# Kernel optimization log

Measured on AMD Instinct MI355X. Metric: run time of the kernel, lower is better.

## Reference

```python
import jax, jax.numpy as jnp
import numpy as np

N, C, E, H, K, GH, L = 50000, 256, 800000, 64, 32, 64, 2
EPS = 1e-8
LN_EPS = 1e-5


def setup_inputs() -> dict:
    key = jax.random.key(0)
    ks = jax.random.split(key, 24)
    s = lambda fan_in: 1.0 / np.sqrt(fan_in)
    inp = {
        "x": jax.random.normal(ks[0], (N, C), jnp.float32),
        "src": jax.random.randint(ks[1], (E,), 0, N),
        "dst": jax.random.randint(ks[2], (E,), 0, N),
        "base_w": jax.random.uniform(ks[3], (E,), jnp.float32),
        # encoder: Linear(C,H) -> ReLU -> Linear(H,H) -> ReLU  (weights stored [in,out])
        "enc_w1": jax.random.normal(ks[4], (C, H), jnp.float32) * s(C),
        "enc_b1": jnp.zeros((H,), jnp.float32),
        "enc_w2": jax.random.normal(ks[5], (H, H), jnp.float32) * s(H),
        "enc_b2": jnp.zeros((H,), jnp.float32),
        # edge gate: Linear(2H, GH) -> ReLU -> Linear(GH, 1) -> sigmoid
        "gate_w1": jax.random.normal(ks[6], (2 * H, GH), jnp.float32) * s(2 * H),
        "gate_b1": jnp.zeros((GH,), jnp.float32),
        "gate_w2": jax.random.normal(ks[7], (GH, 1), jnp.float32) * 0.1,
        "gate_b2": jnp.full((1,), 2.0, jnp.float32),
        # per-layer update MLPs (stacked over L layers): Linear(H,H)->ReLU->Linear(H,H)
        "upd_w1": jax.random.normal(ks[8], (L, H, H), jnp.float32) * s(H),
        "upd_b1": jnp.zeros((L, H), jnp.float32),
        "upd_w2": jax.random.normal(ks[9], (L, H, H), jnp.float32) * s(H),
        "upd_b2": jnp.zeros((L, H), jnp.float32),
        # per-layer LayerNorm params
        "ln_g": jnp.ones((L, H), jnp.float32),
        "ln_b": jnp.zeros((L, H), jnp.float32),
        # node reliability logits
        "rho_raw": jax.random.normal(ks[10], (N,), jnp.float32) * 0.1,
        # toU head: Linear(H, K)
        "toU_w": jax.random.normal(ks[11], (H, K), jnp.float32) * 0.1,
        "toU_b": jnp.ones((K,), jnp.float32),
    }
    return inp


def reference(x, src, dst, base_w,
              enc_w1, enc_b1, enc_w2, enc_b2,
              gate_w1, gate_b1, gate_w2, gate_b2,
              upd_w1, upd_b1, upd_w2, upd_b2,
              ln_g, ln_b, rho_raw, toU_w, toU_b):
    relu = jax.nn.relu
    # node encoder
    h = relu(relu(x @ enc_w1 + enc_b1) @ enc_w2 + enc_b2)  # [N, H]
    rho = jax.nn.sigmoid(rho_raw)                          # [N]
    rho_e = rho[src] * rho[dst]                            # [E]
    for l in range(L):
        h_src = h[src]                                     # [E, H] gather
        h_dst = h[dst]                                     # [E, H] gather
        z = relu(jnp.concatenate([h_src, h_dst], axis=1) @ gate_w1 + gate_b1)
        gate = jax.nn.sigmoid((z @ gate_w2 + gate_b2)[:, 0])  # [E]
        w = base_w * gate * rho_e                           # [E]
        # weighted scatter-add aggregate with degree normalization
        m = jax.ops.segment_sum(w[:, None] * h_src, dst, num_segments=N)  # [N, H]
        deg = jax.ops.segment_sum(w, dst, num_segments=N)                 # [N]
        neigh = m / (deg[:, None] + EPS)
        u = relu(neigh @ upd_w1[l] + upd_b1[l]) @ upd_w2[l] + upd_b2[l]
        pre = h + u
        mean = jnp.mean(pre, axis=-1, keepdims=True)
        var = jnp.var(pre, axis=-1, keepdims=True)
        h = (pre - mean) / jnp.sqrt(var + LN_EPS) * ln_g[l] + ln_b[l]
    U = jax.nn.softplus(h @ toU_w + toU_b)                 # [N, K]
    return U
```

## Files before the change

### kernel.cpp

```cpp
#include <hip/hip_runtime.h>
#include <math.h>


typedef unsigned short ushort_t;
typedef __attribute__((ext_vector_type(8))) short bf16x8;
typedef __attribute__((ext_vector_type(4))) float f32x4;

__device__ __forceinline__ float bf2f(ushort_t u) {
    return __uint_as_float(((unsigned int)u) << 16);
}
__device__ __forceinline__ ushort_t f2bf(float f) {
    unsigned int x = __float_as_uint(f);
    unsigned int lsb = (x >> 16) & 1u;
    x += 0x7fffu + lsb;
    return (ushort_t)(x >> 16);
}

__global__ __launch_bounds__(256) void pack_kernel(
    const float* __restrict__ w1, const float* __restrict__ w2,
    const float* __restrict__ gw1, const float* __restrict__ uw1,
    const float* __restrict__ uw2, const float* __restrict__ tw,
    ushort_t* __restrict__ w1f, ushort_t* __restrict__ w2f,
    ushort_t* __restrict__ g1f, ushort_t* __restrict__ u1f,
    ushort_t* __restrict__ u2f, ushort_t* __restrict__ tuf) {
    int t = blockIdx.x * 256 + threadIdx.x;
    if (t < 16384) {
        int i = t & 7, l = (t >> 3) & 63, kb = (t >> 9) & 7, nt = t >> 12;
        int k = kb * 32 + (l >> 4) * 8 + i, n = nt * 16 + (l & 15);
        w1f[t] = f2bf(w1[(size_t)k * 64 + n]);
    }
    if (t < 4096) {
        int i = t & 7, l = (t >> 3) & 63, kb = (t >> 9) & 1, nt = t >> 10;
        int k = kb * 32 + (l >> 4) * 8 + i, n = nt * 16 + (l & 15);
        w2f[t] = f2bf(w2[(size_t)k * 64 + n]);
    }
    if (t < 8192) {
        int i = t & 7, l = (t >> 3) & 63, kb = (t >> 9) & 1, j = t >> 10;
        int part = j >> 2, nt = j & 3;
        int k = part * 64 + kb * 32 + (l >> 4) * 8 + i, n = nt * 16 + (l & 15);
        g1f[t] = f2bf(gw1[(size_t)k * 64 + n]);
    }
    if (t < 8192) {
        int i = t & 7, l = (t >> 3) & 63, kb = (t >> 9) & 1;
        int nt = (t >> 10) & 3, lay = t >> 12;
        int k = kb * 32 + (l >> 4) * 8 + i, n = nt * 16 + (l & 15);
        u1f[t] = f2bf(uw1[(size_t)lay * 4096 + (size_t)k * 64 + n]);
        u2f[t] = f2bf(uw2[(size_t)lay * 4096 + (size_t)k * 64 + n]);
    }
    if (t < 2048) {
        int i = t & 7, l = (t >> 3) & 63, kb = (t >> 9) & 1, nt = t >> 10;
        int k = kb * 32 + (l >> 4) * 8 + i, n = nt * 16 + (l & 15);
        tuf[t] = f2bf(tw[(size_t)k * 32 + n]);
    }
}

__global__ __launch_bounds__(256) void enc_kernel(
    const float* __restrict__ x, const ushort_t* __restrict__ w1f,
    const float* __restrict__ b1, const ushort_t* __restrict__ w2f,
    const float* __restrict__ b2, const ushort_t* __restrict__ g1f,
    const float* __restrict__ gb1,
    ushort_t* __restrict__ ahb, float* __restrict__ bbuf, int N) {
    __shared__ ushort_t xls[4][16][264];
    __shared__ ushort_t tls[4][16][72];
    const int tid  = threadIdx.x;
    const int lane = tid & 63;
    const int w    = tid >> 6;
    const int m    = lane & 15;
    const int g    = lane >> 4;
    const int rbase = blockIdx.x * 64;
    for (int p = tid; p < 64 * 64; p += 256) {
        int row = p >> 6, k4 = p & 63;
        int grow = rbase + row;
        float4 v = (grow < N) ? *(const float4*)(x + (size_t)grow * 256 + k4 * 4)
                              : make_float4(0.f, 0.f, 0.f, 0.f);
        unsigned int p0 = (unsigned int)f2bf(v.x) | ((unsigned int)f2bf(v.y) << 16);
        unsigned int p1 = (unsigned int)f2bf(v.z) | ((unsigned int)f2bf(v.w) << 16);
        *(uint2*)&xls[row >> 4][row & 15][k4 * 4] = make_uint2(p0, p1);
    }
    __syncthreads();
    f32x4 acc[4] = {{0,0,0,0},{0,0,0,0},{0,0,0,0},{0,0,0,0}};
    #pragma unroll
    for (int kb = 0; kb < 8; ++kb) {
        bf16x8 a = *(const bf16x8*)&xls[w][m][kb * 32 + g * 8];
        #pragma unroll
        for (int nt = 0; nt < 4; ++nt) {
            bf16x8 b = *(const bf16x8*)(w1f + (((size_t)nt * 8 + kb) * 64 + lane) * 8);
            acc[nt] = __builtin_amdgcn_mfma_f32_16x16x32_bf16(a, b, acc[nt], 0, 0, 0);
        }
    }
    #pragma unroll
    for (int nt = 0; nt < 4; ++nt) {
        float bb1 = b1[nt * 16 + m];
        #pragma unroll
        for (int r = 0; r < 4; ++r) {
            float tv = fmaxf(acc[nt][r] + bb1, 0.f);
            tls[w][g * 4 + r][nt * 16 + m] = f2bf(tv);
        }
    }
    f32x4 acc2[4] = {{0,0,0,0},{0,0,0,0},{0,0,0,0},{0,0,0,0}};
    #pragma unroll
    for (int kb = 0; kb < 2; ++kb) {
        bf16x8 a2 = *(const bf16x8*)&tls[w][m][kb * 32 + g * 8];
        #pragma unroll
        for (int nt = 0; nt < 4; ++nt) {
            bf16x8 b = *(const bf16x8*)(w2f + (((size_t)nt * 2 + kb) * 64 + lane) * 8);
            acc2[nt] = __builtin_amdgcn_mfma_f32_16x16x32_bf16(a2, b, acc2[nt], 0, 0, 0);
        }
    }
    #pragma unroll
    for (int nt = 0; nt < 4; ++nt) {
        float bb2 = b2[nt * 16 + m];
        #pragma unroll
        for (int r = 0; r < 4; ++r) {
            float hv = fmaxf(acc2[nt][r] + bb2, 0.f);
            int grow = rbase + w * 16 + g * 4 + r;
            ushort_t hb = f2bf(hv);
            tls[w][g * 4 + r][nt * 16 + m] = hb;
            if (grow < N)
                ahb[(size_t)grow * 128 + 64 + nt * 16 + m] = hb;
        }
    }
    f32x4 accp[8] = {{0,0,0,0},{0,0,0,0},{0,0,0,0},{0,0,0,0},
                     {0,0,0,0},{0,0,0,0},{0,0,0,0},{0,0,0,0}};
    #pragma unroll
    for (int kb = 0; kb < 2; ++kb) {
        bf16x8 a3 = *(const bf16x8*)&tls[w][m][kb * 32 + g * 8];
        #pragma unroll
        for (int j = 0; j < 8; ++j) {
            bf16x8 b = *(const bf16x8*)(g1f + (((size_t)j * 2 + kb) * 64 + lane) * 8);
            accp[j] = __builtin_amdgcn_mfma_f32_16x16x32_bf16(a3, b, accp[j], 0, 0, 0);
        }
    }
    #pragma unroll
    for (int nt = 0; nt < 4; ++nt) {
        float gbl = gb1[nt * 16 + m];
        #pragma unroll
        for (int r = 0; r < 4; ++r) {
            int grow = rbase + w * 16 + g * 4 + r;
            if (grow < N) {
                ahb[(size_t)grow * 128 + nt * 16 + m] = f2bf(accp[nt][r] + gbl);
                bbuf[(size_t)grow * 64 + nt * 16 + m] = accp[nt + 4][r];
            }
        }
    }
}

__global__ __launch_bounds__(256) void hist_kernel(
    const int* __restrict__ dst, int* __restrict__ cnt,
    int* __restrict__ rank, int E) {
    for (int e = blockIdx.x * blockDim.x + threadIdx.x; e < E;
         e += gridDim.x * blockDim.x)
        rank[e] = atomicAdd(&cnt[dst[e]], 1);
}

__global__ __launch_bounds__(256) void scan1_kernel(
    const int* __restrict__ cnt, int* __restrict__ bsum, int N) {
    __shared__ int red[256];
    int i = blockIdx.x * 256 + threadIdx.x;
    red[threadIdx.x] = (i < N) ? cnt[i] : 0;
    __syncthreads();
    for (int off = 128; off > 0; off >>= 1) {
        if (threadIdx.x < off) red[threadIdx.x] += red[threadIdx.x + off];
        __syncthreads();
    }
    if (threadIdx.x == 0) bsum[blockIdx.x] = red[0];
}

__global__ __launch_bounds__(1024) void scan2_kernel(
    int* __restrict__ bsum, int nb) {
    __shared__ int s[1024];
    int v = (threadIdx.x < nb) ? bsum[threadIdx.x] : 0;
    s[threadIdx.x] = v;
    __syncthreads();
    for (int off = 1; off < 1024; off <<= 1) {
        int t = (threadIdx.x >= off) ? s[threadIdx.x - off] : 0;
        __syncthreads();
        s[threadIdx.x] += t;
        __syncthreads();
    }
    if (threadIdx.x < nb) bsum[threadIdx.x] = s[threadIdx.x] - v;
}

__global__ __launch_bounds__(256) void scan3_kernel(
    const int* __restrict__ cnt, const int* __restrict__ bsum,
    int* __restrict__ row_ptr, int N) {
    __shared__ int s[256];
    int i = blockIdx.x * 256 + threadIdx.x;
    int v = (i < N) ? cnt[i] : 0;
    s[threadIdx.x] = v;
    __syncthreads();
    for (int off = 1; off < 256; off <<= 1) {
        int t = (threadIdx.x >= off) ? s[threadIdx.x - off] : 0;
        __syncthreads();
        s[threadIdx.x] += t;
        __syncthreads();
    }
    if (i < N) row_ptr[i] = bsum[blockIdx.x] + s[threadIdx.x] - v;
    if (i == N - 1) row_ptr[N] = bsum[blockIdx.x] + s[threadIdx.x];
}

__global__ __launch_bounds__(256) void scatter_kernel(
    const int* __restrict__ src, const int* __restrict__ dst,
    const float* __restrict__ base_w, const float* __restrict__ rr,
    const int* __restrict__ row_ptr, const int* __restrict__ rank,
    int2* __restrict__ recs, int E) {
    for (int e = blockIdx.x * blockDim.x + threadIdx.x; e < E;
         e += gridDim.x * blockDim.x) {
        int s = src[e], d = dst[e];
        int pos = row_ptr[d] + rank[e];
        float rs = 1.f / (1.f + __expf(-rr[s]));
        float rd = 1.f / (1.f + __expf(-rr[d]));
        float c = base_w[e] * rs * rd;
        recs[pos] = make_int2(s, __float_as_int(c));
    }
}

__global__ __launch_bounds__(256) void gateagg_kernel(
    const int* __restrict__ row_ptr, const int2* __restrict__ recs,
    const ushort_t* __restrict__ ahb, const float* __restrict__ bb,
    const float* __restrict__ gw2, const float* __restrict__ gb2,
    ushort_t* __restrict__ nb, int N) {
    const int lane = threadIdx.x & 63;
    const int sub  = lane & 15;
    const int grp  = lane >> 4;
    const float4 gv = ((const float4*)gw2)[sub];
    const float gb = gb2[0];
    const int wid  = blockIdx.x * (blockDim.x >> 6) + (threadIdx.x >> 6);
    const int nw   = gridDim.x * (blockDim.x >> 6);
    for (int n = wid; n < N; n += nw) {
        const int beg = row_ptr[n], end = row_ptr[n + 1];
        const float4 bv = *(const float4*)(bb + (size_t)n * 64 + sub * 4);
        float m0 = 0.f, m1 = 0.f, m2 = 0.f, m3 = 0.f, dacc = 0.f;
        int i = beg + grp;
        for (; i + 4 < end; i += 8) {
            int2 rA = recs[i];
            int2 rB = recs[i + 4];
            const ushort_t* rowA = ahb + (size_t)rA.x * 128;
            const ushort_t* rowB = ahb + (size_t)rB.x * 128;
            ushort4 avA = *(const ushort4*)(rowA + sub * 4);
            ushort4 hvA = *(const ushort4*)(rowA + 64 + sub * 4);
            ushort4 avB = *(const ushort4*)(rowB + sub * 4);
            ushort4 hvB = *(const ushort4*)(rowB + 64 + sub * 4);
            float tA = fmaxf(bf2f(avA.x) + bv.x, 0.f) * gv.x
                     + fmaxf(bf2f(avA.y) + bv.y, 0.f) * gv.y
                     + fmaxf(bf2f(avA.z) + bv.z, 0.f) * gv.z
                     + fmaxf(bf2f(avA.w) + bv.w, 0.f) * gv.w;
            float tB = fmaxf(bf2f(avB.x) + bv.x, 0.f) * gv.x
                     + fmaxf(bf2f(avB.y) + bv.y, 0.f) * gv.y
                     + fmaxf(bf2f(avB.z) + bv.z, 0.f) * gv.z
                     + fmaxf(bf2f(avB.w) + bv.w, 0.f) * gv.w;
            #pragma unroll
            for (int o = 8; o > 0; o >>= 1) {
                tA += __shfl_xor(tA, o, 64);
                tB += __shfl_xor(tB, o, 64);
            }
            float wA = __int_as_float(rA.y) / (1.f + __expf(-(tA + gb)));
            float wB = __int_as_float(rB.y) / (1.f + __expf(-(tB + gb)));
            m0 = fmaf(wA, bf2f(hvA.x), m0); m0 = fmaf(wB, bf2f(hvB.x), m0);
            m1 = fmaf(wA, bf2f(hvA.y), m1); m1 = fmaf(wB, bf2f(hvB.y), m1);
            m2 = fmaf(wA, bf2f(hvA.z), m2); m2 = fmaf(wB, bf2f(hvB.z), m2);
            m3 = fmaf(wA, bf2f(hvA.w), m3); m3 = fmaf(wB, bf2f(hvB.w), m3);
            dacc += wA + wB;
        }
        if (i < end) {
            int2 r = recs[i];
            const ushort_t* row = ahb + (size_t)r.x * 128;
            ushort4 av = *(const ushort4*)(row + sub * 4);
            ushort4 hv = *(const ushort4*)(row + 64 + sub * 4);
            float t = fmaxf(bf2f(av.x) + bv.x, 0.f) * gv.x
                    + fmaxf(bf2f(av.y) + bv.y, 0.f) * gv.y
                    + fmaxf(bf2f(av.z) + bv.z, 0.f) * gv.z
                    + fmaxf(bf2f(av.w) + bv.w, 0.f) * gv.w;
            #pragma unroll
            for (int o = 8; o > 0; o >>= 1) t += __shfl_xor(t, o, 64);
            float w = __int_as_float(r.y) / (1.f + __expf(-(t + gb)));
            m0 = fmaf(w, bf2f(hv.x), m0);
            m1 = fmaf(w, bf2f(hv.y), m1);
            m2 = fmaf(w, bf2f(hv.z), m2);
            m3 = fmaf(w, bf2f(hv.w), m3);
            dacc += w;
        }
        #pragma unroll
        for (int o = 16; o < 64; o <<= 1) {
            m0 += __shfl_xor(m0, o, 64);
            m1 += __shfl_xor(m1, o, 64);
            m2 += __shfl_xor(m2, o, 64);
            m3 += __shfl_xor(m3, o, 64);
            dacc += __shfl_xor(dacc, o, 64);
        }
        if (lane < 16) {
            float dg = dacc + 1e-8f;
            ushort4 o4;
            o4.x = f2bf(m0 / dg);
            o4.y = f2bf(m1 / dg);
            o4.z = f2bf(m2 / dg);
            o4.w = f2bf(m3 / dg);
            *(ushort4*)(nb + (size_t)n * 64 + sub * 4) = o4;
        }
    }
}

template <int MODE>
__global__ __launch_bounds__(256) void upd_kernel(
    const ushort_t* __restrict__ nb,
    const ushort_t* __restrict__ u1f, const float* __restrict__ b1,
    const ushort_t* __restrict__ u2f, const float* __restrict__ b2,
    const float* __restrict__ lng, const float* __restrict__ lnb,
    const ushort_t* __restrict__ g1f, const float* __restrict__ gb1,
    ushort_t* __restrict__ ahb, float* __restrict__ bbuf,
    const ushort_t* __restrict__ tuf, const float* __restrict__ tub,
    float* __restrict__ U, int N) {
    __shared__ ushort_t tls[4][16][72];
    const int tid  = threadIdx.x;
    const int lane = tid & 63;
    const int w    = tid >> 6;
    const int m_   = lane & 15;
    const int g    = lane >> 4;
    const int rbase = blockIdx.x * 64;
    const int arow = rbase + w * 16 + m_;
    const bool rowok = arow < N;
    f32x4 acc[4] = {{0,0,0,0},{0,0,0,0},{0,0,0,0},{0,0,0,0}};
    #pragma unroll
    for (int kb = 0; kb < 2; ++kb) {
        bf16x8 a = {0, 0, 0, 0, 0, 0, 0, 0};
        if (rowok) a = *(const bf16x8*)(nb + (size_t)arow * 64 + kb * 32 + g * 8);
        #pragma unroll
        for (int nt = 0; nt < 4; ++nt) {
            bf16x8 b = *(const bf16x8*)(u1f + (((size_t)nt * 2 + kb) * 64 + lane) * 8);
            acc[nt] = __builtin_amdgcn_mfma_f32_16x16x32_bf16(a, b, acc[nt], 0, 0, 0);
        }
    }
    #pragma unroll
    for (int nt = 0; nt < 4; ++nt) {
        float bb1 = b1[nt * 16 + m_];
        #pragma unroll
        for (int r = 0; r < 4; ++r)
            tls[w][g * 4 + r][nt * 16 + m_] = f2bf(fmaxf(acc[nt][r] + bb1, 0.f));
    }
    f32x4 acc2[4] = {{0,0,0,0},{0,0,0,0},{0,0,0,0},{0,0,0,0}};
    #pragma unroll
    for (int kb = 0; kb < 2; ++kb) {
        bf16x8 a2 = *(const bf16x8*)&tls[w][m_][kb * 32 + g * 8];
        #pragma unroll
        for (int nt = 0; nt < 4; ++nt) {
            bf16x8 b = *(const bf16x8*)(u2f + (((size_t)nt * 2 + kb) * 64 + lane) * 8);
            acc2[nt] = __builtin_amdgcn_mfma_f32_16x16x32_bf16(a2, b, acc2[nt], 0, 0, 0);
        }
    }
    float hn_reg[4][4];
    #pragma unroll
    for (int r = 0; r < 4; ++r) {
        const int grow = rbase + w * 16 + g * 4 + r;
        float pre[4];
        float s1 = 0.f, s2 = 0.f;
        #pragma unroll
        for (int nt = 0; nt < 4; ++nt) {
            float hv = (grow < N)
                ? bf2f(ahb[(size_t)grow * 128 + 64 + nt * 16 + m_]) : 0.f;
            pre[nt] = acc2[nt][r] + b2[nt * 16 + m_] + hv;
            s1 += pre[nt];
            s2 += pre[nt] * pre[nt];
        }
        #pragma unroll
        for (int o = 1; o < 16; o <<= 1) {
            s1 += __shfl_xor(s1, o, 64);
            s2 += __shfl_xor(s2, o, 64);
        }
        float mean = s1 * (1.0f / 64.0f);
        float var  = s2 * (1.0f / 64.0f) - mean * mean;
        float rinv = rsqrtf(var + 1e-5f);
        #pragma unroll
        for (int nt = 0; nt < 4; ++nt) {
            float hn = (pre[nt] - mean) * rinv * lng[nt * 16 + m_] + lnb[nt * 16 + m_];
            hn_reg[r][nt] = hn;
            tls[w][g * 4 + r][nt * 16 + m_] = f2bf(hn);
        }
    }
    if (MODE == 0) {
        #pragma unroll
        for (int nt = 0; nt < 4; ++nt) {
            #pragma unroll
            for (int r = 0; r < 4; ++r) {
                int grow = rbase + w * 16 + g * 4 + r;
                if (grow < N)
                    ahb[(size_t)grow * 128 + 64 + nt * 16 + m_] = f2bf(hn_reg[r][nt]);
            }
        }
        f32x4 accp[8] = {{0,0,0,0},{0,0,0,0},{0,0,0,0},{0,0,0,0},
                         {0,0,0,0},{0,0,0,0},{0,0,0,0},{0,0,0,0}};
        #pragma unroll
        for (int kb = 0; kb < 2; ++kb) {
            bf16x8 a3 = *(const bf16x8*)&tls[w][m_][kb * 32 + g * 8];
            #pragma unroll
            for (int j = 0; j < 8; ++j) {
                bf16x8 b = *(const bf16x8*)(g1f + (((size_t)j * 2 + kb) * 64 + lane) * 8);
                accp[j] = __builtin_amdgcn_mfma_f32_16x16x32_bf16(a3, b, accp[j], 0, 0, 0);
            }
        }
        #pragma unroll
        for (int nt = 0; nt < 4; ++nt) {
            float gbl = gb1[nt * 16 + m_];
            #pragma unroll
            for (int r = 0; r < 4; ++r) {
                int grow = rbase + w * 16 + g * 4 + r;
                if (grow < N) {
                    ahb[(size_t)grow * 128 + nt * 16 + m_] = f2bf(accp[nt][r] + gbl);
                    bbuf[(size_t)grow * 64 + nt * 16 + m_] = accp[nt + 4][r];
                }
            }
        }
    } else {
        f32x4 accu[2] = {{0,0,0,0},{0,0,0,0}};
        #pragma unroll
        for (int kb = 0; kb < 2; ++kb) {
            bf16x8 a3 = *(const bf16x8*)&tls[w][m_][kb * 32 + g * 8];
            #pragma unroll
            for (int nt = 0; nt < 2; ++nt) {
                bf16x8 b = *(const bf16x8*)(tuf + (((size_t)nt * 2 + kb) * 64 + lane) * 8);
                accu[nt] = __builtin_amdgcn_mfma_f32_16x16x32_bf16(a3, b, accu[nt], 0, 0, 0);
            }
        }
        #pragma unroll
        for (int nt = 0; nt < 2; ++nt) {
            float tb = tub[nt * 16 + m_];
            #pragma unroll
            for (int r = 0; r < 4; ++r) {
                int grow = rbase + w * 16 + g * 4 + r;
                if (grow < N) {
                    float av = accu[nt][r] + tb;
                    float sp = av > 0.f ? av + log1pf(__expf(-av))
                                        : log1pf(__expf(av));
                    U[(size_t)grow * 32 + nt * 16 + m_] = sp;
                }
            }
        }
    }
}

extern "C" void kernel_launch(void* const* d_in, const int* in_sizes, int n_in,
                              void* d_out, int out_size, void* d_ws, size_t ws_size,
                              hipStream_t stream) {
    const float* x       = (const float*)d_in[0];
    const int*   src     = (const int*)d_in[1];
    const int*   dst     = (const int*)d_in[2];
    const float* base_w  = (const float*)d_in[3];
    const float* enc_w1  = (const float*)d_in[4];
    const float* enc_b1  = (const float*)d_in[5];
    const float* enc_w2  = (const float*)d_in[6];
    const float* enc_b2  = (const float*)d_in[7];
    const float* gate_w1 = (const float*)d_in[8];
    const float* gate_b1 = (const float*)d_in[9];
    const float* gate_w2 = (const float*)d_in[10];
    const float* gate_b2 = (const float*)d_in[11];
    const float* upd_w1  = (const float*)d_in[12];
    const float* upd_b1  = (const float*)d_in[13];
    const float* upd_w2  = (const float*)d_in[14];
    const float* upd_b2  = (const float*)d_in[15];
    const float* ln_g    = (const float*)d_in[16];
    const float* ln_b    = (const float*)d_in[17];
    const float* rho_raw = (const float*)d_in[18];
    const float* toU_w   = (const float*)d_in[19];
    const float* toU_b   = (const float*)d_in[20];

    const int N = in_sizes[18];
    const int E = in_sizes[1];
    const int nsb = (N + 255) / 256;

    float* ws  = (float*)d_ws;
    size_t off = 0;
    ushort_t* ahb = (ushort_t*)(ws + off); off += (size_t)N * 64;
    float* bb  = ws + off; off += (size_t)N * 64;
    ushort_t* nb = (ushort_t*)(ws + off); off += (size_t)N * 32;
    int* row_ptr = (int*)(ws + off); off += (size_t)((N + 1 + 3) & ~3);
    int* cnt     = (int*)(ws + off); off += (size_t)((N + 3) & ~3);
    int* bsum    = (int*)(ws + off); off += (size_t)((nsb + 3) & ~3);
    int* rank    = (int*)(ws + off); off += (size_t)E;
    int2* recs   = (int2*)(ws + off); off += (size_t)E * 2;
    ushort_t* w1f = (ushort_t*)(ws + off); off += 8192;
    ushort_t* w2f = (ushort_t*)(ws + off); off += 2048;
    ushort_t* g1f = (ushort_t*)(ws + off); off += 4096;
    ushort_t* u1f = (ushort_t*)(ws + off); off += 4096;
    ushort_t* u2f = (ushort_t*)(ws + off); off += 4096;
    ushort_t* tuf = (ushort_t*)(ws + off); off += 1024;

    pack_kernel<<<64, 256, 0, stream>>>(enc_w1, enc_w2, gate_w1, upd_w1, upd_w2,
                                        toU_w, w1f, w2f, g1f, u1f, u2f, tuf);
    const int nblk64 = (N + 63) / 64;
    enc_kernel<<<nblk64, 256, 0, stream>>>(x, w1f, enc_b1, w2f, enc_b2,
                                           g1f, gate_b1, ahb, bb, N);

    hipMemsetAsync(cnt, 0, (size_t)N * sizeof(int), stream);
    hist_kernel<<<(E + 255) / 256, 256, 0, stream>>>(dst, cnt, rank, E);
    scan1_kernel<<<nsb, 256, 0, stream>>>(cnt, bsum, N);
    scan2_kernel<<<1, 1024, 0, stream>>>(bsum, nsb);
    scan3_kernel<<<nsb, 256, 0, stream>>>(cnt, bsum, row_ptr, N);
    scatter_kernel<<<(E + 255) / 256, 256, 0, stream>>>(src, dst, base_w, rho_raw,
                                                        row_ptr, rank, recs, E);

    gateagg_kernel<<<2048, 256, 0, stream>>>(row_ptr, recs, ahb, bb,
                                             gate_w2, gate_b2, nb, N);
    upd_kernel<0><<<nblk64, 256, 0, stream>>>(
        nb, u1f, upd_b1, u2f, upd_b2, ln_g, ln_b,
        g1f, gate_b1, ahb, bb, tuf, toU_b, (float*)d_out, N);

    gateagg_kernel<<<2048, 256, 0, stream>>>(row_ptr, recs, ahb, bb,
                                             gate_w2, gate_b2, nb, N);
    upd_kernel<1><<<nblk64, 256, 0, stream>>>(
        nb, u1f + 4096, upd_b1 + 64, u2f + 4096, upd_b2 + 64,
        ln_g + 64, ln_b + 64,
        g1f, gate_b1, ahb, bb, tuf, toU_b, (float*)d_out, N);
}
```

Baseline: 213.3 us.

## Split node tile across waves by output columns and stage stores through LDS

The encoder and update kernels now process 16 nodes per block instead of 64. Each of the four waves computes one 16-column slice of the output rather than a full 16-row tile, with LDS exchanges and block barriers between stages and a cross-wave LayerNorm reduction done through shared memory. Global writes of h, the gate projections and bbuf are staged through LDS so they go out as row-contiguous vector stores instead of scattered 2-byte stores. The intent is 4x more blocks for better occupancy and wider global stores. The cost is extra barriers, redundant A-operand LDS reads across waves, and W operands reloaded per block.

New measurement: 200.0 us. 6.2% less time.

```diff
diff --git a/kernel.cpp b/kernel.cpp
--- a/kernel.cpp
+++ b/kernel.cpp
@@ -60,87 +60,93 @@
     const float* __restrict__ b2, const ushort_t* __restrict__ g1f,
     const float* __restrict__ gb1,
     ushort_t* __restrict__ ahb, float* __restrict__ bbuf, int N) {
-    __shared__ ushort_t xls[4][16][264];
-    __shared__ ushort_t tls[4][16][72];
+    __shared__ ushort_t xls[16][264];
+    __shared__ ushort_t tls[16][72];
+    __shared__ ushort_t hls[16][72];
+    __shared__ ushort_t als[16][72];
+    __shared__ float    bls[16][68];
     const int tid  = threadIdx.x;
     const int lane = tid & 63;
     const int w    = tid >> 6;
     const int m    = lane & 15;
     const int g    = lane >> 4;
-    const int rbase = blockIdx.x * 64;
-    for (int p = tid; p < 64 * 64; p += 256) {
-        int row = p >> 6, k4 = p & 63;
-        int grow = rbase + row;
+    const int rbase = blockIdx.x * 16;
+    for (int p = tid; p < 16 * 64; p += 256) {
+        int row = p >> 6, k4 = p & 63, grow = rbase + row;
         float4 v = (grow < N) ? *(const float4*)(x + (size_t)grow * 256 + k4 * 4)
                               : make_float4(0.f, 0.f, 0.f, 0.f);
         unsigned int p0 = (unsigned int)f2bf(v.x) | ((unsigned int)f2bf(v.y) << 16);
         unsigned int p1 = (unsigned int)f2bf(v.z) | ((unsigned int)f2bf(v.w) << 16);
-        *(uint2*)&xls[row >> 4][row & 15][k4 * 4] = make_uint2(p0, p1);
-    }
-    __syncthreads();
-    f32x4 acc[4] = {{0,0,0,0},{0,0,0,0},{0,0,0,0},{0,0,0,0}};
+        *(uint2*)&xls[row][k4 * 4] = make_uint2(p0, p1);
+    }
+    __syncthreads();
+    f32x4 acc = {0, 0, 0, 0};
     #pragma unroll
     for (int kb = 0; kb < 8; ++kb) {
-        bf16x8 a = *(const bf16x8*)&xls[w][m][kb * 32 + g * 8];
-        #pragma unroll
-        for (int nt = 0; nt < 4; ++nt) {
-            bf16x8 b = *(const bf16x8*)(w1f + (((size_t)nt * 8 + kb) * 64 + lane) * 8);
-            acc[nt] = __builtin_amdgcn_mfma_f32_16x16x32_bf16(a, b, acc[nt], 0, 0, 0);
-        }
-    }
-    #pragma unroll
-    for (int nt = 0; nt < 4; ++nt) {
-        float bb1 = b1[nt * 16 + m];
-        #pragma unroll
-        for (int r = 0; r < 4; ++r) {
-            float tv = fmaxf(acc[nt][r] + bb1, 0.f);
-            tls[w][g * 4 + r][nt * 16 + m] = f2bf(tv);
-        }
-    }
-    f32x4 acc2[4] = {{0,0,0,0},{0,0,0,0},{0,0,0,0},{0,0,0,0}};
+        bf16x8 a = *(const bf16x8*)&xls[m][kb * 32 + g * 8];
+        bf16x8 b = *(const bf16x8*)(w1f + (((size_t)w * 8 + kb) * 64 + lane) * 8);
+        acc = __builtin_amdgcn_mfma_f32_16x16x32_bf16(a, b, acc, 0, 0, 0);
+    }
+    {
+        float bb1 = b1[w * 16 + m];
+        #pragma unroll
+        for (int r = 0; r < 4; ++r)
+            tls[g * 4 + r][w * 16 + m] = f2bf(fmaxf(acc[r] + bb1, 0.f));
+    }
+    __syncthreads();
+    f32x4 acc2 = {0, 0, 0, 0};
     #pragma unroll
     for (int kb = 0; kb < 2; ++kb) {
-        bf16x8 a2 = *(const bf16x8*)&tls[w][m][kb * 32 + g * 8];
-        #pragma unroll
-        for (int nt = 0; nt < 4; ++nt) {
-            bf16x8 b = *(const bf16x8*)(w2f + (((size_t)nt * 2 + kb) * 64 + lane) * 8);
-            acc2[nt] = __builtin_amdgcn_mfma_f32_16x16x32_bf16(a2, b, acc2[nt], 0, 0, 0);
-        }
-    }
-    #pragma unroll
-    for (int nt = 0; nt < 4; ++nt) {
-        float bb2 = b2[nt * 16 + m];
-        #pragma unroll
-        for (int r = 0; r < 4; ++r) {
-            float hv = fmaxf(acc2[nt][r] + bb2, 0.f);
-            int grow = rbase + w * 16 + g * 4 + r;
-            ushort_t hb = f2bf(hv);
-            tls[w][g * 4 + r][nt * 16 + m] = hb;
-            if (grow < N)
-                ahb[(size_t)grow * 128 + 64 + nt * 16 + m] = hb;
-        }
-    }
-    f32x4 accp[8] = {{0,0,0,0},{0,0,0,0},{0,0,0,0},{0,0,0,0},
-                     {0,0,0,0},{0,0,0,0},{0,0,0,0},{0,0,0,0}};
+        bf16x8 a2 = *(const bf16x8*)&tls[m][kb * 32 + g * 8];
+        bf16x8 b = *(const bf16x8*)(w2f + (((size_t)w * 2 + kb) * 64 + lane) * 8);
+        acc2 = __builtin_amdgcn_mfma_f32_16x16x32_bf16(a2, b, acc2, 0, 0, 0);
+    }
+    {
+        float bb2 = b2[w * 16 + m];
+        #pragma unroll
+        for (int r = 0; r < 4; ++r)
+            hls[g * 4 + r][w * 16 + m] = f2bf(fmaxf(acc2[r] + bb2, 0.f));
+    }
+    __syncthreads();
+    {
+        int row = tid >> 4, c4 = tid & 15, grow = rbase + row;
+        if (grow < N)
+            *(ushort4*)(ahb + (size_t)grow * 128 + 64 + c4 * 4) =
+                *(const ushort4*)&hls[row][c4 * 4];
+    }
+    f32x4 p0 = {0, 0, 0, 0}, p1 = {0, 0, 0, 0};
     #pragma unroll
     for (int kb = 0; kb < 2; ++kb) {
-        bf16x8 a3 = *(const bf16x8*)&tls[w][m][kb * 32 + g * 8];
-        #pragma unroll
-        for (int j = 0; j < 8; ++j) {
-            bf16x8 b = *(const bf16x8*)(g1f + (((size_t)j * 2 + kb) * 64 + lane) * 8);
-            accp[j] = __builtin_amdgcn_mfma_f32_16x16x32_bf16(a3, b, accp[j], 0, 0, 0);
-        }
-    }
-    #pragma unroll
-    for (int nt = 0; nt < 4; ++nt) {
-        float gbl = gb1[nt * 16 + m];
+        bf16x8 a3 = *(const bf16x8*)&hls[m][kb * 32 + g * 8];
+        bf16x8 b0 = *(const bf16x8*)(g1f + (((size_t)(2 * w) * 2 + kb) * 64 + lane) * 8);
+        bf16x8 b1v = *(const bf16x8*)(g1f + (((size_t)(2 * w + 1) * 2 + kb) * 64 + lane) * 8);
+        p0 = __builtin_amdgcn_mfma_f32_16x16x32_bf16(a3, b0, p0, 0, 0, 0);
+        p1 = __builtin_amdgcn_mfma_f32_16x16x32_bf16(a3, b1v, p1, 0, 0, 0);
+    }
+    if (w < 2) {
+        int j0 = 2 * w, j1 = 2 * w + 1;
+        float gb0 = gb1[j0 * 16 + m], gb1v = gb1[j1 * 16 + m];
         #pragma unroll
         for (int r = 0; r < 4; ++r) {
-            int grow = rbase + w * 16 + g * 4 + r;
-            if (grow < N) {
-                ahb[(size_t)grow * 128 + nt * 16 + m] = f2bf(accp[nt][r] + gbl);
-                bbuf[(size_t)grow * 64 + nt * 16 + m] = accp[nt + 4][r];
-            }
+            als[g * 4 + r][j0 * 16 + m] = f2bf(p0[r] + gb0);
+            als[g * 4 + r][j1 * 16 + m] = f2bf(p1[r] + gb1v);
+        }
+    } else {
+        int j0 = 2 * w - 4, j1 = 2 * w - 3;
+        #pragma unroll
+        for (int r = 0; r < 4; ++r) {
+            bls[g * 4 + r][j0 * 16 + m] = p0[r];
+            bls[g * 4 + r][j1 * 16 + m] = p1[r];
+        }
+    }
+    __syncthreads();
+    {
+        int row = tid >> 4, c4 = tid & 15, grow = rbase + row;
+        if (grow < N) {
+            *(ushort4*)(ahb + (size_t)grow * 128 + c4 * 4) =
+                *(const ushort4*)&als[row][c4 * 4];
+            *(float4*)(bbuf + (size_t)grow * 64 + c4 * 4) =
+                *(const float4*)&bls[row][c4 * 4];
         }
     }
 }
@@ -310,127 +316,144 @@
     ushort_t* __restrict__ ahb, float* __restrict__ bbuf,
     const ushort_t* __restrict__ tuf, const float* __restrict__ tub,
     float* __restrict__ U, int N) {
-    __shared__ ushort_t tls[4][16][72];
+    __shared__ ushort_t xn[16][72];
+    __shared__ ushort_t hls[16][72];
+    __shared__ ushort_t tls[16][72];
+    __shared__ ushort_t als[16][72];
+    __shared__ float    bls[16][68];
+    __shared__ float    sred[16][4][2];
     const int tid  = threadIdx.x;
     const int lane = tid & 63;
     const int w    = tid >> 6;
     const int m_   = lane & 15;
     const int g    = lane >> 4;
-    const int rbase = blockIdx.x * 64;
-    const int arow = rbase + w * 16 + m_;
-    const bool rowok = arow < N;
-    f32x4 acc[4] = {{0,0,0,0},{0,0,0,0},{0,0,0,0},{0,0,0,0}};
+    const int rbase = blockIdx.x * 16;
+    {
+        int row = tid >> 4, c4 = tid & 15, grow = rbase + row;
+        ushort4 z; z.x = z.y = z.z = z.w = 0;
+        ushort4 nv = (grow < N) ? *(const ushort4*)(nb + (size_t)grow * 64 + c4 * 4) : z;
+        ushort4 hv = (grow < N) ? *(const ushort4*)(ahb + (size_t)grow * 128 + 64 + c4 * 4) : z;
+        *(ushort4*)&xn[row][c4 * 4] = nv;
+        *(ushort4*)&hls[row][c4 * 4] = hv;
+    }
+    __syncthreads();
+    f32x4 acc = {0, 0, 0, 0};
     #pragma unroll
     for (int kb = 0; kb < 2; ++kb) {
-        bf16x8 a = {0, 0, 0, 0, 0, 0, 0, 0};
-        if (rowok) a = *(const bf16x8*)(nb + (size_t)arow * 64 + kb * 32 + g * 8);
-        #pragma unroll
-        for (int nt = 0; nt < 4; ++nt) {
-            bf16x8 b = *(const bf16x8*)(u1f + (((size_t)nt * 2 + kb) * 64 + lane) * 8);
-            acc[nt] = __builtin_amdgcn_mfma_f32_16x16x32_bf16(a, b, acc[nt], 0, 0, 0);
-        }
-    }
-    #pragma unroll
-    for (int nt = 0; nt < 4; ++nt) {
-        float bb1 = b1[nt * 16 + m_];
+        bf16x8 a = *(const bf16x8*)&xn[m_][kb * 32 + g * 8];
+        bf16x8 b = *(const bf16x8*)(u1f + (((size_t)w * 2 + kb) * 64 + lane) * 8);
+        acc = __builtin_amdgcn_mfma_f32_16x16x32_bf16(a, b, acc, 0, 0, 0);
+    }
+    {
+        float bb1 = b1[w * 16 + m_];
         #pragma unroll
         for (int r = 0; r < 4; ++r)
-            tls[w][g * 4 + r][nt * 16 + m_] = f2bf(fmaxf(acc[nt][r] + bb1, 0.f));
-    }
-    f32x4 acc2[4] = {{0,0,0,0},{0,0,0,0},{0,0,0,0},{0,0,0,0}};
+            tls[g * 4 + r][w * 16 + m_] = f2bf(fmaxf(acc[r] + bb1, 0.f));
+    }
+    __syncthreads();
+    f32x4 acc2 = {0, 0, 0, 0};
     #pragma unroll
     for (int kb = 0; kb < 2; ++kb) {
-        bf16x8 a2 = *(const bf16x8*)&tls[w][m_][kb * 32 + g * 8];
-        #pragma unroll
-        for (int nt = 0; nt < 4; ++nt) {
-            bf16x8 b = *(const bf16x8*)(u2f + (((size_t)nt * 2 + kb) * 64 + lane) * 8);
-            acc2[nt] = __builtin_amdgcn_mfma_f32_16x16x32_bf16(a2, b, acc2[nt], 0, 0, 0);
-        }
-    }
-    float hn_reg[4][4];
-    #pragma unroll
-    for (int r = 0; r < 4; ++r) {
-        const int grow = rbase + w * 16 + g * 4 + r;
-        float pre[4];
-        float s1 = 0.f, s2 = 0.f;
-        #pragma unroll
-        for (int nt = 0; nt < 4; ++nt) {
-            float hv = (grow < N)
-                ? bf2f(ahb[(size_t)grow * 128 + 64 + nt * 16 + m_]) : 0.f;
-            pre[nt] = acc2[nt][r] + b2[nt * 16 + m_] + hv;
-            s1 += pre[nt];
-            s2 += pre[nt] * pre[nt];
-        }
-        #pragma unroll
-        for (int o = 1; o < 16; o <<= 1) {
-            s1 += __shfl_xor(s1, o, 64);
-            s2 += __shfl_xor(s2, o, 64);
-        }
-        float mean = s1 * (1.0f / 64.0f);
-        float var  = s2 * (1.0f / 64.0f) - mean * mean;
-        float rinv = rsqrtf(var + 1e-5f);
-        #pragma unroll
-        for (int nt = 0; nt < 4; ++nt) {
-            float hn = (pre[nt] - mean) * rinv * lng[nt * 16 + m_] + lnb[nt * 16 + m_];
-            hn_reg[r][nt] = hn;
-            tls[w][g * 4 + r][nt * 16 + m_] = f2bf(hn);
-        }
-    }
+        bf16x8 a2 = *(const bf16x8*)&tls[m_][kb * 32 + g * 8];
+        bf16x8 b = *(const bf16x8*)(u2f + (((size_t)w * 2 + kb) * 64 + lane) * 8);
+        acc2 = __builtin_amdgcn_mfma_f32_16x16x32_bf16(a2, b, acc2, 0, 0, 0);
+    }
+    float pre[4];
+    {
+        float bb2 = b2[w * 16 + m_];
+        #pragma unroll
+        for (int r = 0; r < 4; ++r) {
+            pre[r] = acc2[r] + bb2 + bf2f(hls[g * 4 + r][w * 16 + m_]);
+            float s1 = pre[r], s2 = pre[r] * pre[r];
+            #pragma unroll
+            for (int o = 1; o < 16; o <<= 1) {
+                s1 += __shfl_xor(s1, o, 64);
+                s2 += __shfl_xor(s2, o, 64);
+            }
+            if (m_ == 0) {
+                sred[g * 4 + r][w][0] = s1;
+                sred[g * 4 + r][w][1] = s2;
+            }
+        }
+    }
+    __syncthreads();
+    {
+        float lg = lng[w * 16 + m_], lb = lnb[w * 16 + m_];
+        #pragma unroll
+        for (int r = 0; r < 4; ++r) {
+            int row = g * 4 + r;
+            float s1 = (sred[row][0][0] + sred[row][1][0])
+                     + (sred[row][2][0] + sred[row][3][0]);
+            float s2 = (sred[row][0][1] + sred[row][1][1])
+                     + (sred[row][2][1] + sred[row][3][1]);
+            float mean = s1 * (1.0f / 64.0f);
+            float var  = s2 * (1.0f / 64.0f) - mean * mean;
+            float rinv = rsqrtf(var + 1e-5f);
+            float hn = (pre[r] - mean) * rinv * lg + lb;
+            tls[row][w * 16 + m_] = f2bf(hn);
+        }
+    }
+    __syncthreads();
     if (MODE == 0) {
-        #pragma unroll
-        for (int nt = 0; nt < 4; ++nt) {
+        {
+            int row = tid >> 4, c4 = tid & 15, grow = rbase + row;
+            if (grow < N)
+                *(ushort4*)(ahb + (size_t)grow * 128 + 64 + c4 * 4) =
+                    *(const ushort4*)&tls[row][c4 * 4];
+        }
+        f32x4 p0 = {0, 0, 0, 0}, p1 = {0, 0, 0, 0};
+        #pragma unroll
+        for (int kb = 0; kb < 2; ++kb) {
+            bf16x8 a3 = *(const bf16x8*)&tls[m_][kb * 32 + g * 8];
+            bf16x8 b0 = *(const bf16x8*)(g1f + (((size_t)(2 * w) * 2 + kb) * 64 + lane) * 8);
+            bf16x8 b1v = *(const bf16x8*)(g1f + (((size_t)(2 * w + 1) * 2 + kb) * 64 + lane) * 8);
+            p0 = __builtin_amdgcn_mfma_f32_16x16x32_bf16(a3, b0, p0, 0, 0, 0);
+            p1 = __builtin_amdgcn_mfma_f32_16x16x32_bf16(a3, b1v, p1, 0, 0, 0);
+        }
+        if (w < 2) {
+            int j0 = 2 * w, j1 = 2 * w + 1;
+            float gb0 = gb1[j0 * 16 + m_], gb1v = gb1[j1 * 16 + m_];
             #pragma unroll
             for (int r = 0; r < 4; ++r) {
-                int grow = rbase + w * 16 + g * 4 + r;
-                if (grow < N)
-                    ahb[(size_t)grow * 128 + 64 + nt * 16 + m_] = f2bf(hn_reg[r][nt]);
-            }
-        }
-        f32x4 accp[8] = {{0,0,0,0},{0,0,0,0},{0,0,0,0},{0,0,0,0},
-                         {0,0,0,0},{0,0,0,0},{0,0,0,0},{0,0,0,0}};
-        #pragma unroll
-        for (int kb = 0; kb < 2; ++kb) {
-            bf16x8 a3 = *(const bf16x8*)&tls[w][m_][kb * 32 + g * 8];
-            #pragma unroll
-            for (int j = 0; j < 8; ++j) {
-                bf16x8 b = *(const bf16x8*)(g1f + (((size_t)j * 2 + kb) * 64 + lane) * 8);
-                accp[j] = __builtin_amdgcn_mfma_f32_16x16x32_bf16(a3, b, accp[j], 0, 0, 0);
-            }
-        }
-        #pragma unroll
-        for (int nt = 0; nt < 4; ++nt) {
-            float gbl = gb1[nt * 16 + m_];
+                als[g * 4 + r][j0 * 16 + m_] = f2bf(p0[r] + gb0);
+                als[g * 4 + r][j1 * 16 + m_] = f2bf(p1[r] + gb1v);
+            }
+        } else {
+            int j0 = 2 * w - 4, j1 = 2 * w - 3;
             #pragma unroll
             for (int r = 0; r < 4; ++r) {
-                int grow = rbase + w * 16 + g * 4 + r;
+                bls[g * 4 + r][j0 * 16 + m_] = p0[r];
+                bls[g * 4 + r][j1 * 16 + m_] = p1[r];
+            }
+        }
+        __syncthreads();
+        {
+            int row = tid >> 4, c4 = tid & 15, grow = rbase + row;
+            if (grow < N) {
+                *(ushort4*)(ahb + (size_t)grow * 128 + c4 * 4) =
+                    *(const ushort4*)&als[row][c4 * 4];
+                *(float4*)(bbuf + (size_t)grow * 64 + c4 * 4) =
+                    *(const float4*)&bls[row][c4 * 4];
+            }
+        }
+    } else {
+        if (w < 2) {
+            f32x4 au = {0, 0, 0, 0};
+            #pragma unroll
+            for (int kb = 0; kb < 2; ++kb) {
+                bf16x8 a3 = *(const bf16x8*)&tls[m_][kb * 32 + g * 8];
+                bf16x8 b = *(const bf16x8*)(tuf + (((size_t)w * 2 + kb) * 64 + lane) * 8);
+                au = __builtin_amdgcn_mfma_f32_16x16x32_bf16(a3, b, au, 0, 0, 0);
+            }
+            float tb = tub[w * 16 + m_];
+            #pragma unroll
+            for (int r = 0; r < 4; ++r) {
+                int grow = rbase + g * 4 + r;
                 if (grow < N) {
-                    ahb[(size_t)grow * 128 + nt * 16 + m_] = f2bf(accp[nt][r] + gbl);
-                    bbuf[(size_t)grow * 64 + nt * 16 + m_] = accp[nt + 4][r];
-                }
-            }
-        }
-    } else {
-        f32x4 accu[2] = {{0,0,0,0},{0,0,0,0}};
-        #pragma unroll
-        for (int kb = 0; kb < 2; ++kb) {
-            bf16x8 a3 = *(const bf16x8*)&tls[w][m_][kb * 32 + g * 8];
-            #pragma unroll
-            for (int nt = 0; nt < 2; ++nt) {
-                bf16x8 b = *(const bf16x8*)(tuf + (((size_t)nt * 2 + kb) * 64 + lane) * 8);
-                accu[nt] = __builtin_amdgcn_mfma_f32_16x16x32_bf16(a3, b, accu[nt], 0, 0, 0);
-            }
-        }
-        #pragma unroll
-        for (int nt = 0; nt < 2; ++nt) {
-            float tb = tub[nt * 16 + m_];
-            #pragma unroll
-            for (int r = 0; r < 4; ++r) {
-                int grow = rbase + w * 16 + g * 4 + r;
-                if (grow < N) {
-                    float av = accu[nt][r] + tb;
+                    float av = au[r] + tb;
                     float sp = av > 0.f ? av + log1pf(__expf(-av))
                                         : log1pf(__expf(av));
-                    U[(size_t)grow * 32 + nt * 16 + m_] = sp;
+                    U[(size_t)grow * 32 + w * 16 + m_] = sp;
                 }
             }
         }
@@ -485,8 +508,8 @@
 
     pack_kernel<<<64, 256, 0, stream>>>(enc_w1, enc_w2, gate_w1, upd_w1, upd_w2,
                                         toU_w, w1f, w2f, g1f, u1f, u2f, tuf);
-    const int nblk64 = (N + 63) / 64;
-    enc_kernel<<<nblk64, 256, 0, stream>>>(x, w1f, enc_b1, w2f, enc_b2,
+    const int nblk16 = (N + 15) / 16;
+    enc_kernel<<<nblk16, 256, 0, stream>>>(x, w1f, enc_b1, w2f, enc_b2,
                                            g1f, gate_b1, ahb, bb, N);
 
     hipMemsetAsync(cnt, 0, (size_t)N * sizeof(int), stream);
@@ -499,13 +522,13 @@
 
     gateagg_kernel<<<2048, 256, 0, stream>>>(row_ptr, recs, ahb, bb,
                                              gate_w2, gate_b2, nb, N);
-    upd_kernel<0><<<nblk64, 256, 0, stream>>>(
+    upd_kernel<0><<<nblk16, 256, 0, stream>>>(
         nb, u1f, upd_b1, u2f, upd_b2, ln_g, ln_b,
         g1f, gate_b1, ahb, bb, tuf, toU_b, (float*)d_out, N);
 
     gateagg_kernel<<<2048, 256, 0, stream>>>(row_ptr, recs, ahb, bb,
                                              gate_w2, gate_b2, nb, N);
-    upd_kernel<1><<<nblk64, 256, 0, stream>>>(
+    upd_kernel<1><<<nblk16, 256, 0, stream>>>(
         nb, u1f + 4096, upd_b1 + 64, u2f + 4096, upd_b2 + 64,
         ln_g + 64, ln_b + 64,
         g1f, gate_b1, ahb, bb, tuf, toU_b, (float*)d_out, N);
```
